# Kernel tuning notes

Measured on AMD Instinct MI355X. Metric: run time of the kernel, lower is better.

## Reference

```python
import jax, jax.numpy as jnp
import numpy as np

B, IN, OUT, L, R = 8192, 4096, 4096, 4, 128


def setup_inputs() -> dict:
    key = jax.random.key(0)
    ks = jax.random.split(key, 6)
    scale = 1.0 / np.sqrt(IN)
    return {
        "h_in": jax.random.normal(ks[0], (B, IN), dtype=jnp.float32),
        "S1s": jax.random.normal(ks[1], (L, IN, R), dtype=jnp.float32) * scale,
        "S2s": jax.random.normal(ks[2], (L, R, OUT), dtype=jnp.float32) * scale,
        "U1s": jax.random.normal(ks[3], (L, R, OUT), dtype=jnp.float32) / np.sqrt(R),
        "U2s": jax.random.normal(ks[4], (L, IN, R), dtype=jnp.float32) / np.sqrt(R),
        "bias": jax.random.normal(ks[5], (OUT,), dtype=jnp.float32) * scale,
    }


def reference(h_in, S1s, S2s, U1s, U2s, bias):
    l = S1s.shape[0]
    # term 1: x @ S1_i @ U1_i ; sketch to rank r then expand to out
    t1 = jnp.einsum("bi,lir->lbr", h_in, S1s)          # (l, B, r)
    y1 = jnp.einsum("lbr,lro->bo", t1, U1s)             # (B, out)
    # term 2: x @ U2_i @ S2_i
    t2 = jnp.einsum("bi,lir->lbr", h_in, U2s)          # (l, B, r)
    y2 = jnp.einsum("lbr,lro->bo", t2, S2s)             # (B, out)
    out = (y1 + y2) / (2.0 * l) + bias
    return out
```

## Files before the change

### kernel.cpp

```cpp
#include <hip/hip_runtime.h>


using bf16x8 = __attribute__((ext_vector_type(8))) __bf16;
using f32x4  = __attribute__((ext_vector_type(4))) float;

__device__ __forceinline__ unsigned short f2bf(float f) {
    union { float f; unsigned u; } c; c.f = f;
    unsigned u = c.u;
    return (unsigned short)((u + 0x7FFFu + ((u >> 16) & 1u)) >> 16);
}

__device__ __forceinline__ void gload_lds16(const void* g, void* l) {
    __builtin_amdgcn_global_load_lds((const __attribute__((address_space(1))) void*)g,
                                     (__attribute__((address_space(3))) void*)l,
                                     16, 0, 0);
}

__global__ void cvt_f32_to_bf16(const float4* __restrict__ src, ushort4* __restrict__ dst, int n4) {
    int i = blockIdx.x * blockDim.x + threadIdx.x;
    int stride = gridDim.x * blockDim.x;
    for (; i < n4; i += stride) {
        float4 v = src[i];
        ushort4 o;
        o.x = f2bf(v.x); o.y = f2bf(v.y); o.z = f2bf(v.z); o.w = f2bf(v.w);
        dst[i] = o;
    }
}

__global__ void pack_transpose(const float* __restrict__ p0, const float* __restrict__ p1,
                               unsigned short* __restrict__ dst,
                               int srcStride, int dstStride, long perT, long dstTOff) {
    const int t = blockIdx.z;
    const float* src = (t < 4) ? (p0 + (long)t * perT) : (p1 + (long)(t - 4) * perT);
    unsigned short* d = dst + (long)t * dstTOff;
    const int r0 = blockIdx.x * 32, c0 = blockIdx.y * 32;
    __shared__ float tile[32][33];
    const int tx = threadIdx.x & 31, ty = threadIdx.x >> 5;
#pragma unroll
    for (int j = 0; j < 4; ++j) {
        int rr = ty + j * 8;
        tile[rr][tx] = src[(long)(r0 + rr) * srcStride + c0 + tx];
    }
    __syncthreads();
#pragma unroll
    for (int j = 0; j < 4; ++j) {
        int cc = ty + j * 8;
        d[(long)(c0 + cc) * dstStride + r0 + tx] = f2bf(tile[tx][cc]);
    }
}

template <bool OUT_BF16>
__global__ __launch_bounds__(256) void gemm_bt(const unsigned short* __restrict__ A,
                                               const unsigned short* __restrict__ Bt,
                                               void* __restrict__ Cout,
                                               const float* __restrict__ bias,
                                               int M, int N, int K, float scale) {
    __shared__ unsigned short lA[128 * 32];
    __shared__ unsigned short lB[128 * 32];
    const int tid = threadIdx.x;
    const int wave = tid >> 6, lane = tid & 63;
    const int m0 = blockIdx.y * 128, n0 = blockIdx.x * 128;
    const int wm = wave >> 1, wn = wave & 1;

    f32x4 acc[4][4] = {};

    const unsigned short* gA = A + (size_t)(m0 + wave * 32 + (lane >> 2)) * K + (lane & 3) * 8;
    const unsigned short* gB = Bt + (size_t)(n0 + wave * 32 + (lane >> 2)) * K + (lane & 3) * 8;
    unsigned short* lA0 = &lA[(wave * 32) * 32];
    unsigned short* lB0 = &lB[(wave * 32) * 32];

    const unsigned short* pa = &lA[(wm * 64 + (lane & 15)) * 32 + (lane >> 4) * 8];
    const unsigned short* pb = &lB[(wn * 64 + (lane & 15)) * 32 + (lane >> 4) * 8];

    for (int kt = 0; kt < K; kt += 32) {
        gload_lds16(gA, lA0);
        gload_lds16(gA + (size_t)16 * K, lA0 + 16 * 32);
        gload_lds16(gB, lB0);
        gload_lds16(gB + (size_t)16 * K, lB0 + 16 * 32);
        __syncthreads();
        bf16x8 av[4], bv[4];
#pragma unroll
        for (int i = 0; i < 4; ++i) {
            av[i] = *(const bf16x8*)(pa + i * 16 * 32);
            bv[i] = *(const bf16x8*)(pb + i * 16 * 32);
        }
#pragma unroll
        for (int i = 0; i < 4; ++i)
#pragma unroll
            for (int j = 0; j < 4; ++j)
                acc[i][j] = __builtin_amdgcn_mfma_f32_16x16x32_bf16(av[i], bv[j], acc[i][j], 0, 0, 0);
        __syncthreads();
        gA += 32; gB += 32;
    }

    const int row0 = m0 + wm * 64, col0 = n0 + wn * 64;
    const int lr = (lane >> 4) * 4, lc = lane & 15;
    if (OUT_BF16) {
        unsigned short* Cb = (unsigned short*)Cout;
#pragma unroll
        for (int i = 0; i < 4; ++i)
#pragma unroll
            for (int j = 0; j < 4; ++j) {
                int col = col0 + j * 16 + lc;
#pragma unroll
                for (int q = 0; q < 4; ++q) {
                    int row = row0 + i * 16 + lr + q;
                    Cb[(size_t)row * N + col] = f2bf(acc[i][j][q]);
                }
            }
    } else {
        float* Cf = (float*)Cout;
#pragma unroll
        for (int i = 0; i < 4; ++i)
#pragma unroll
            for (int j = 0; j < 4; ++j) {
                int col = col0 + j * 16 + lc;
                float bv = bias[col];
#pragma unroll
                for (int q = 0; q < 4; ++q) {
                    int row = row0 + i * 16 + lr + q;
                    Cf[(size_t)row * N + col] = acc[i][j][q] * scale + bv;
                }
            }
    }
}

extern "C" void kernel_launch(void* const* d_in, const int* in_sizes, int n_in,
                              void* d_out, int out_size, void* d_ws, size_t ws_size,
                              hipStream_t stream) {
    const float* h_in = (const float*)d_in[0];
    const float* S1s  = (const float*)d_in[1];
    const float* S2s  = (const float*)d_in[2];
    const float* U1s  = (const float*)d_in[3];
    const float* U2s  = (const float*)d_in[4];
    const float* bias = (const float*)d_in[5];
    float* out = (float*)d_out;

    constexpr int B = 8192, IN = 4096, OUTD = 4096, R = 128;
    constexpr int NC = 1024;

    char* ws = (char*)d_ws;
    unsigned short* hB    = (unsigned short*)ws;
    unsigned short* AcatT = (unsigned short*)(ws + ((size_t)64 << 20));
    unsigned short* BcatT = (unsigned short*)(ws + ((size_t)72 << 20));
    unsigned short* T     = (unsigned short*)(ws + ((size_t)80 << 20));

    cvt_f32_to_bf16<<<2048, 256, 0, stream>>>((const float4*)h_in, (ushort4*)hB, B * IN / 4);

    pack_transpose<<<dim3(IN / 32, R / 32, 8), 256, 0, stream>>>(
        S1s, U2s, AcatT, R, IN, (long)IN * R, (long)R * IN);
    pack_transpose<<<dim3(R / 32, OUTD / 32, 8), 256, 0, stream>>>(
        U1s, S2s, BcatT, OUTD, NC, (long)R * OUTD, (long)R);

    gemm_bt<true><<<dim3(NC / 128, B / 128), 256, 0, stream>>>(hB, AcatT, (void*)T, nullptr,
                                                               B, NC, IN, 1.0f);
    gemm_bt<false><<<dim3(OUTD / 128, B / 128), 256, 0, stream>>>(T, BcatT, (void*)out, bias,
                                                                  B, OUTD, NC, 0.125f);
}
```

Measured before the change: 448.2 us.

## Replace simple GEMM with 8-wave double-buffered pipelined MFMA kernel

Replaces the 128x128, 256-thread GEMM with a 512-thread kernel using 256xBN tiles, a 64-deep K step, double-buffered LDS with XOR-swizzled layout, and interleaved async global-to-LDS staging between MFMA bursts with raised wave priority. It also adds workgroup index swizzling for L2 locality and nontemporal output stores. The aim is to hide memory latency and cut LDS bank conflicts and per-iteration barrier stalls, at the cost of much higher register and LDS pressure and hand-tuned waitcnt ordering that must stay correct.

```diff
diff --git a/kernel.cpp b/kernel.cpp
--- a/kernel.cpp
+++ b/kernel.cpp
@@ -49,80 +49,154 @@
     }
 }
 
-template <bool OUT_BF16>
-__global__ __launch_bounds__(256) void gemm_bt(const unsigned short* __restrict__ A,
-                                               const unsigned short* __restrict__ Bt,
-                                               void* __restrict__ Cout,
-                                               const float* __restrict__ bias,
-                                               int M, int N, int K, float scale) {
-    __shared__ unsigned short lA[128 * 32];
-    __shared__ unsigned short lB[128 * 32];
+
+#define SB() __builtin_amdgcn_s_barrier()
+#define WVM(n) { asm volatile("s_waitcnt vmcnt(" #n ")" ::: "memory"); __builtin_amdgcn_sched_barrier(0); }
+#define WLG() { asm volatile("s_waitcnt lgkmcnt(0)" ::: "memory"); __builtin_amdgcn_sched_barrier(0); }
+
+template <int BN, bool OUT_BF16>
+__global__ __launch_bounds__(512, 2) void gemm8p(const unsigned short* __restrict__ A,
+                                                 const unsigned short* __restrict__ Bt,
+                                                 void* __restrict__ Cout,
+                                                 const float* __restrict__ bias,
+                                                 int M, int N, int K, float scale) {
+    constexpr int BM = 256;
+    constexpr int NF = BN / 64;
+    constexpr int WN = BN / 4;
+    constexpr int BHALF = BN * 64;
+    constexpr int BUFB = 32768 + BN * 128;
+    __shared__ __align__(128) char smem[2 * BUFB];
+
     const int tid = threadIdx.x;
-    const int wave = tid >> 6, lane = tid & 63;
-    const int m0 = blockIdx.y * 128, n0 = blockIdx.x * 128;
-    const int wm = wave >> 1, wn = wave & 1;
-
-    f32x4 acc[4][4] = {};
-
-    const unsigned short* gA = A + (size_t)(m0 + wave * 32 + (lane >> 2)) * K + (lane & 3) * 8;
-    const unsigned short* gB = Bt + (size_t)(n0 + wave * 32 + (lane >> 2)) * K + (lane & 3) * 8;
-    unsigned short* lA0 = &lA[(wave * 32) * 32];
-    unsigned short* lB0 = &lB[(wave * 32) * 32];
-
-    const unsigned short* pa = &lA[(wm * 64 + (lane & 15)) * 32 + (lane >> 4) * 8];
-    const unsigned short* pb = &lB[(wn * 64 + (lane & 15)) * 32 + (lane >> 4) * 8];
-
-    for (int kt = 0; kt < K; kt += 32) {
-        gload_lds16(gA, lA0);
-        gload_lds16(gA + (size_t)16 * K, lA0 + 16 * 32);
-        gload_lds16(gB, lB0);
-        gload_lds16(gB + (size_t)16 * K, lB0 + 16 * 32);
-        __syncthreads();
-        bf16x8 av[4], bv[4];
-#pragma unroll
-        for (int i = 0; i < 4; ++i) {
-            av[i] = *(const bf16x8*)(pa + i * 16 * 32);
-            bv[i] = *(const bf16x8*)(pb + i * 16 * 32);
+    const int w = tid >> 6, lane = tid & 63;
+    const int wm = w >> 2, wn = w & 3;
+
+    const int nwg = gridDim.x;
+    const int wg = blockIdx.x;
+    const int swz = (wg & 7) * (nwg >> 3) + (wg >> 3);
+    const int nbn = N / BN;
+    const int m0 = (swz / nbn) * BM, n0 = (swz % nbn) * BN;
+
+    const int NT = K >> 6;
+
+    const int rl = lane >> 3;
+    const int csw = (lane & 7) ^ rl;
+    const unsigned short* gA = A + (size_t)(m0 + w * 8 + rl) * K + csw * 8;
+    const unsigned short* gB = Bt + (size_t)(n0 + w * 8 + rl) * K + csw * 8;
+
+    const int aRB = wm * 16384 + (lane & 15) * 128;
+    const int bRB = 32768 + (wn >> 1) * BHALF + ((wn & 1) * WN + (lane & 15)) * 128;
+    const int ch0 = (((lane >> 4) + 0) ^ (lane & 7)) << 4;
+    const int ch1 = (((lane >> 4) + 4) ^ (lane & 7)) << 4;
+
+    f32x4 acc[8][NF] = {};
+    bf16x8 av[8][2], bv[NF][2];
+
+#define STAGE_A(tt, h) {                                                              \
+        const unsigned short* g_ = gA + (size_t)((h) * 128) * K + (size_t)(tt) * 64;  \
+        char* l_ = smem + ((tt) & 1) * BUFB + (h) * 16384 + w * 1024;                 \
+        gload_lds16(g_, l_);                                                          \
+        gload_lds16(g_ + (size_t)64 * K, l_ + 8192); }
+
+#define STAGE_B(tt, h) {                                                                   \
+        const unsigned short* g_ = gB + (size_t)((h) * (BN / 2)) * K + (size_t)(tt) * 64;  \
+        char* l_ = smem + ((tt) & 1) * BUFB + 32768 + (h) * BHALF + w * 1024;              \
+        gload_lds16(g_, l_);                                                               \
+        if (BN == 256) gload_lds16(g_ + (size_t)64 * K, l_ + 8192); }
+
+#define LOADA(c, base) {                                                            \
+        _Pragma("unroll")                                                           \
+        for (int f_ = 0; f_ < 4; ++f_) {                                            \
+            const char* p_ = smem + (c) * BUFB + aRB + ((base) + f_) * 2048;        \
+            av[(base) + f_][0] = *(const bf16x8*)(p_ + ch0);                        \
+            av[(base) + f_][1] = *(const bf16x8*)(p_ + ch1);                        \
+        } }
+
+#define LOADB(c, base) {                                                            \
+        _Pragma("unroll")                                                           \
+        for (int f_ = 0; f_ < NF / 2; ++f_) {                                       \
+            const char* p_ = smem + (c) * BUFB + bRB + ((base) + f_) * 2048;        \
+            bv[(base) + f_][0] = *(const bf16x8*)(p_ + ch0);                        \
+            bv[(base) + f_][1] = *(const bf16x8*)(p_ + ch1);                        \
+        } }
+
+#define BURST(mb, nb) {                                                             \
+        __builtin_amdgcn_s_setprio(1);                                              \
+        _Pragma("unroll")                                                           \
+        for (int f_ = 0; f_ < 4; ++f_)                                              \
+            _Pragma("unroll")                                                       \
+            for (int g_ = 0; g_ < NF / 2; ++g_) {                                   \
+                acc[(mb) + f_][(nb) + g_] = __builtin_amdgcn_mfma_f32_16x16x32_bf16(\
+                    av[(mb) + f_][0], bv[(nb) + g_][0], acc[(mb) + f_][(nb) + g_], 0, 0, 0); \
+                acc[(mb) + f_][(nb) + g_] = __builtin_amdgcn_mfma_f32_16x16x32_bf16(\
+                    av[(mb) + f_][1], bv[(nb) + g_][1], acc[(mb) + f_][(nb) + g_], 0, 0, 0); \
+            }                                                                       \
+        __builtin_amdgcn_s_setprio(0); }
+
+    STAGE_A(0, 0); STAGE_A(0, 1);
+    STAGE_B(0, 0); STAGE_B(0, 1);
+    STAGE_A(1, 0); STAGE_A(1, 1);
+
+    for (int t = 0; t < NT - 1; ++t) {
+        const int c = t & 1;
+        WVM(4); SB();
+        LOADA(c, 0); LOADB(c, 0);
+        STAGE_B(t + 1, 0);
+        SB(); WLG();
+        BURST(0, 0);
+        SB();
+        LOADA(c, 4); LOADB(c, NF / 2);
+        STAGE_B(t + 1, 1);
+        SB(); WLG();
+        BURST(4, 0);
+        SB();
+        if (t + 2 < NT) STAGE_A(t + 2, 0);
+        SB();
+        BURST(0, NF / 2);
+        SB();
+        if (t + 2 < NT) STAGE_A(t + 2, 1);
+        SB();
+        BURST(4, NF / 2);
+    }
+    {
+        const int c = (NT - 1) & 1;
+        WVM(0); SB();
+        LOADA(c, 0); LOADB(c, 0);
+        SB(); WLG();
+        BURST(0, 0); SB();
+        LOADA(c, 4); LOADB(c, NF / 2);
+        SB(); WLG();
+        BURST(4, 0); SB();
+        BURST(0, NF / 2); SB();
+        BURST(4, NF / 2);
+    }
+
+    const int lc = lane & 15, lr = (lane >> 4) * 4;
+#pragma unroll
+    for (int fm = 0; fm < 8; ++fm)
+#pragma unroll
+        for (int fn = 0; fn < NF; ++fn) {
+            const int col = n0 + wn * WN + fn * 16 + lc;
+            const int row = m0 + wm * 128 + fm * 16 + lr;
+            if constexpr (OUT_BF16) {
+                unsigned short* Cb = (unsigned short*)Cout;
+#pragma unroll
+                for (int q = 0; q < 4; ++q)
+                    Cb[(size_t)(row + q) * N + col] = f2bf(acc[fm][fn][q]);
+            } else {
+                float* Cf = (float*)Cout;
+                const float bb = bias[col];
+#pragma unroll
+                for (int q = 0; q < 4; ++q)
+                    __builtin_nontemporal_store(acc[fm][fn][q] * scale + bb,
+                                                &Cf[(size_t)(row + q) * N + col]);
+            }
         }
-#pragma unroll
-        for (int i = 0; i < 4; ++i)
-#pragma unroll
-            for (int j = 0; j < 4; ++j)
-                acc[i][j] = __builtin_amdgcn_mfma_f32_16x16x32_bf16(av[i], bv[j], acc[i][j], 0, 0, 0);
-        __syncthreads();
-        gA += 32; gB += 32;
-    }
-
-    const int row0 = m0 + wm * 64, col0 = n0 + wn * 64;
-    const int lr = (lane >> 4) * 4, lc = lane & 15;
-    if (OUT_BF16) {
-        unsigned short* Cb = (unsigned short*)Cout;
-#pragma unroll
-        for (int i = 0; i < 4; ++i)
-#pragma unroll
-            for (int j = 0; j < 4; ++j) {
-                int col = col0 + j * 16 + lc;
-#pragma unroll
-                for (int q = 0; q < 4; ++q) {
-                    int row = row0 + i * 16 + lr + q;
-                    Cb[(size_t)row * N + col] = f2bf(acc[i][j][q]);
-                }
-            }
-    } else {
-        float* Cf = (float*)Cout;
-#pragma unroll
-        for (int i = 0; i < 4; ++i)
-#pragma unroll
-            for (int j = 0; j < 4; ++j) {
-                int col = col0 + j * 16 + lc;
-                float bv = bias[col];
-#pragma unroll
-                for (int q = 0; q < 4; ++q) {
-                    int row = row0 + i * 16 + lr + q;
-                    Cf[(size_t)row * N + col] = acc[i][j][q] * scale + bv;
-                }
-            }
-    }
+#undef STAGE_A
+#undef STAGE_B
+#undef LOADA
+#undef LOADB
+#undef BURST
 }
 
 extern "C" void kernel_launch(void* const* d_in, const int* in_sizes, int n_in,
@@ -152,8 +226,8 @@
     pack_transpose<<<dim3(R / 32, OUTD / 32, 8), 256, 0, stream>>>(
         U1s, S2s, BcatT, OUTD, NC, (long)R * OUTD, (long)R);
 
-    gemm_bt<true><<<dim3(NC / 128, B / 128), 256, 0, stream>>>(hB, AcatT, (void*)T, nullptr,
-                                                               B, NC, IN, 1.0f);
-    gemm_bt<false><<<dim3(OUTD / 128, B / 128), 256, 0, stream>>>(T, BcatT, (void*)out, bias,
-                                                                  B, OUTD, NC, 0.125f);
-}
+    gemm8p<128, true><<<dim3((B / 256) * (NC / 128)), 512, 0, stream>>>(
+        hB, AcatT, (void*)T, nullptr, B, NC, IN, 1.0f);
+    gemm8p<256, false><<<dim3((B / 256) * (OUTD / 256)), 512, 0, stream>>>(
+        T, BcatT, (void*)out, bias, B, OUTD, NC, 0.125f);
+}
```

New measurement: 402.8 us. -10.1%, faster.
